# Performance work log

Measured on AMD Instinct MI355X. Metric: run time of the kernel, lower is better.

Reference implementation:

```python
import jax, jax.numpy as jnp
import numpy as np

B, T, N, D, TXT, TE, H = 8, 8192, 256, 512, 768, 2048, 8
DH = D // H


def _ln(x, g, b):
    m = jnp.mean(x, axis=-1, keepdims=True)
    v = jnp.mean(jnp.square(x - m), axis=-1, keepdims=True)
    return (x - m) * jax.lax.rsqrt(v + 1e-5) * g + b


def setup_inputs() -> dict:
    key = jax.random.key(0)
    ks = jax.random.split(key, 10)
    s = 0.02  # init scale for weights (zero_module init replaced by small random for a non-trivial baseline)
    return {
        "x": jax.random.normal(ks[0], (B, T, D), jnp.float32),
        "xf": jax.random.normal(ks[1], (B, N, TXT), jnp.float32),
        "emb": jax.random.normal(ks[2], (B, TE), jnp.float32),
        "ln_x_g": jnp.ones((D,), jnp.float32),
        "ln_x_b": jnp.zeros((D,), jnp.float32),
        "ln_t_g": jnp.ones((TXT,), jnp.float32),
        "ln_t_b": jnp.zeros((TXT,), jnp.float32),
        "Wq": jax.random.normal(ks[3], (D, D), jnp.float32) * s,
        "bq": jnp.zeros((D,), jnp.float32),
        "Wk": jax.random.normal(ks[4], (TXT, D), jnp.float32) * s,
        "bk": jnp.zeros((D,), jnp.float32),
        "Wv": jax.random.normal(ks[5], (TXT, D), jnp.float32) * s,
        "bv": jnp.zeros((D,), jnp.float32),
        "emb_W": jax.random.normal(ks[6], (TE, 2 * D), jnp.float32) * s,
        "emb_b": jnp.zeros((2 * D,), jnp.float32),
        "ln_o_g": jnp.ones((D,), jnp.float32),
        "ln_o_b": jnp.zeros((D,), jnp.float32),
        "out_W": jax.random.normal(ks[7], (D, D), jnp.float32) * s,
        "out_b": jnp.zeros((D,), jnp.float32),
    }


def reference(x, xf, emb, ln_x_g, ln_x_b, ln_t_g, ln_t_b, Wq, bq, Wk, bk, Wv, bv,
              emb_W, emb_b, ln_o_g, ln_o_b, out_W, out_b):
    xt = _ln(xf, ln_t_g, ln_t_b)                                  # [B,N,TXT]
    q = jax.nn.softmax((_ln(x, ln_x_g, ln_x_b) @ Wq + bq).reshape(B, T, H, DH), axis=-1)
    k = jax.nn.softmax((xt @ Wk + bk).reshape(B, N, H, DH), axis=-1)
    v = (xt @ Wv + bv).reshape(B, N, H, DH)
    attn = jnp.einsum('bnhd,bnhl->bhdl', k, v)                    # [B,H,DH,DH] kv aggregation
    out = jnp.einsum('bthd,bhdl->bthl', q, attn).reshape(B, T, D)  # [B,T,D]
    # StylizationBlock
    eo = (jax.nn.silu(emb) @ emb_W + emb_b)[:, None, :]           # [B,1,2D]
    scale, shift = jnp.split(eo, 2, axis=2)
    h = _ln(out, ln_o_g, ln_o_b) * (1 + scale) + shift
    h = jax.nn.silu(h) @ out_W + out_b
    return x + h
```

## Files before the change

### kernel.cpp

```cpp
#include <hip/hip_runtime.h>
#include <hip/hip_bf16.h>
#include <math.h>

#define Bc 8
#define Tc 8192
#define NTOK 256
#define Dc 512
#define TXT 768
#define TEc 2048
#define Hc 8
#define DHc 64
#define MROWS (Bc * Tc)

typedef __attribute__((ext_vector_type(8))) short bf16x8v;
typedef __attribute__((ext_vector_type(8))) unsigned short u16x8;
typedef __attribute__((ext_vector_type(4))) unsigned short u16x4;
typedef __attribute__((ext_vector_type(4))) float f32x4;

#define MFMA16(a, b, c) __builtin_amdgcn_mfma_f32_16x16x32_bf16(a, b, c, 0, 0, 0)

__device__ __forceinline__ unsigned short f2bf(float f) {
    __hip_bfloat16 h = __float2bfloat16(f);
    return __builtin_bit_cast(unsigned short, h);
}
__device__ __forceinline__ float bf2f(unsigned short u) {
    unsigned int x = ((unsigned int)u) << 16;
    return __builtin_bit_cast(float, x);
}

typedef __attribute__((address_space(3))) unsigned int lds_u32_t;
typedef __attribute__((address_space(1))) const unsigned int gbl_u32_t;
__device__ __forceinline__ void gload16(const unsigned short* g, short* l) {
    __builtin_amdgcn_global_load_lds((gbl_u32_t*)g, (lds_u32_t*)l, 16, 0, 0);
}

__global__ void __launch_bounds__(256) transpose_kernel(const float* __restrict__ src,
                                                        unsigned short* __restrict__ dst,
                                                        int N, int rs) {
    __shared__ float tile[64][65];
    int k0 = blockIdx.x * 64, n0 = blockIdx.y * 64;
    int tx = threadIdx.x & 63, tq = threadIdx.x >> 6;
#pragma unroll
    for (int i = 0; i < 16; ++i) {
        int kk = tq + i * 4;
        tile[kk][tx] = src[(size_t)(k0 + kk) * N + n0 + tx];
    }
    __syncthreads();
#pragma unroll
    for (int i = 0; i < 16; ++i) {
        int nn = tq + i * 4;
        dst[(size_t)(n0 + nn) * rs + k0 + tx] = f2bf(tile[tx][nn]);
    }
}

__global__ void __launch_bounds__(256) ln_t_kernel(const float* __restrict__ xf,
                                                   const float* __restrict__ g,
                                                   const float* __restrict__ bt,
                                                   unsigned short* __restrict__ xt) {
    int w = threadIdx.x >> 6, l = threadIdx.x & 63;
    int row = blockIdx.x * 4 + w;
    const float* src = xf + (size_t)row * TXT;
    float4 a0 = *(const float4*)&src[l * 12];
    float4 a1 = *(const float4*)&src[l * 12 + 4];
    float4 a2 = *(const float4*)&src[l * 12 + 8];
    float vals[12] = {a0.x, a0.y, a0.z, a0.w, a1.x, a1.y, a1.z, a1.w,
                      a2.x, a2.y, a2.z, a2.w};
    float s = 0.f, ss = 0.f;
#pragma unroll
    for (int j = 0; j < 12; ++j) { s += vals[j]; ss += vals[j] * vals[j]; }
#pragma unroll
    for (int m = 1; m <= 32; m <<= 1) { s += __shfl_xor(s, m); ss += __shfl_xor(ss, m); }
    float mean = s * (1.f / TXT), var = ss * (1.f / TXT) - mean * mean;
    float rs = rsqrtf(var + 1e-5f);
    unsigned short o[12];
#pragma unroll
    for (int j = 0; j < 12; ++j) {
        int c = l * 12 + j;
        o[j] = f2bf((vals[j] - mean) * rs * g[c] + bt[c]);
    }
    unsigned short* dp = xt + (size_t)row * TXT + l * 12;
    *(u16x4*)&dp[0] = *(u16x4*)&o[0];
    *(u16x4*)&dp[4] = *(u16x4*)&o[4];
    *(u16x4*)&dp[8] = *(u16x4*)&o[8];
}

__global__ void __launch_bounds__(256) ln_x_kernel(const float* __restrict__ x,
                                                   const float* __restrict__ g,
                                                   const float* __restrict__ bt,
                                                   unsigned short* __restrict__ A1) {
    int w = threadIdx.x >> 6, l = threadIdx.x & 63;
    int row = blockIdx.x * 4 + w;
    const float* src = x + (size_t)row * Dc;
    float4 a0 = *(const float4*)&src[l * 8];
    float4 a1 = *(const float4*)&src[l * 8 + 4];
    float vals[8] = {a0.x, a0.y, a0.z, a0.w, a1.x, a1.y, a1.z, a1.w};
    float s = 0.f, ss = 0.f;
#pragma unroll
    for (int j = 0; j < 8; ++j) { s += vals[j]; ss += vals[j] * vals[j]; }
#pragma unroll
    for (int m = 1; m <= 32; m <<= 1) { s += __shfl_xor(s, m); ss += __shfl_xor(ss, m); }
    float mean = s * (1.f / Dc), var = ss * (1.f / Dc) - mean * mean;
    float rs = rsqrtf(var + 1e-5f);
    u16x8 o;
#pragma unroll
    for (int j = 0; j < 8; ++j) {
        int c = l * 8 + j;
        o[j] = f2bf((vals[j] - mean) * rs * g[c] + bt[c]);
    }
    *(u16x8*)&A1[(size_t)row * Dc + l * 8] = o;
}

__global__ void __launch_bounds__(256) kvgemm_kernel(
    const unsigned short* __restrict__ xt, const unsigned short* __restrict__ Wkvt,
    const float* __restrict__ bk, const float* __restrict__ bv,
    unsigned short* __restrict__ kbuf, unsigned short* __restrict__ vbuf) {
    __shared__ short lds_s[16384];
    short* Alds = lds_s;
    short* Blds = lds_s + 8192;

    const int tid = threadIdx.x, l = tid & 63, w = tid >> 6;
    const int lr = l & 15, lg = l >> 4;
    int mt = blockIdx.x >> 3, nt = blockIdx.x & 7;
    int row0 = mt * 128, col0 = nt * 128;
    int wrow = (w >> 1) * 64, wcol = (w & 1) * 64;

    f32x4 acc[4][4] = {};
    const int cbase = w * 64 + l;

    for (int ks = 0; ks < 12; ++ks) {
#pragma unroll
        for (int i = 0; i < 4; ++i) {
            int c = i * 256 + cbase;
            int r = c >> 3, kc = c & 7;
            int koff = ks * 64 + ((kc ^ (r & 7)) << 3);
            gload16(xt + (size_t)(row0 + r) * TXT + koff, &Alds[((i * 4 + w) * 64) * 8]);
            gload16(Wkvt + (size_t)(col0 + r) * TXT + koff, &Blds[((i * 4 + w) * 64) * 8]);
        }
        __syncthreads();
#pragma unroll
        for (int kk = 0; kk < 2; ++kk) {
            int kcw = kk * 4 + lg;
            bf16x8v af[4], bfr[4];
#pragma unroll
            for (int i = 0; i < 4; ++i) {
                int r = wrow + i * 16 + lr;
                af[i] = *(bf16x8v*)&Alds[(r * 8 + (kcw ^ (r & 7))) * 8];
            }
#pragma unroll
            for (int j = 0; j < 4; ++j) {
                int n = wcol + j * 16 + lr;
                bfr[j] = *(bf16x8v*)&Blds[(n * 8 + (kcw ^ (n & 7))) * 8];
            }
#pragma unroll
            for (int i = 0; i < 4; ++i)
#pragma unroll
                for (int j = 0; j < 4; ++j)
                    acc[i][j] = MFMA16(af[i], bfr[j], acc[i][j]);
        }
        __syncthreads();
    }

    const bool kHalf = (col0 + wcol) < 512;
    int cj[4];
    float bias[4];
#pragma unroll
    for (int j = 0; j < 4; ++j) {
        cj[j] = col0 + wcol + j * 16 + lr;
        bias[j] = kHalf ? bk[cj[j]] : bv[cj[j] - 512];
    }
#pragma unroll
    for (int i = 0; i < 4; ++i)
#pragma unroll
        for (int reg = 0; reg < 4; ++reg) {
            float v0 = acc[i][0][reg] + bias[0], v1 = acc[i][1][reg] + bias[1];
            float v2 = acc[i][2][reg] + bias[2], v3 = acc[i][3][reg] + bias[3];
            if (kHalf) {
                float m = fmaxf(fmaxf(v0, v1), fmaxf(v2, v3));
                m = fmaxf(m, __shfl_xor(m, 1)); m = fmaxf(m, __shfl_xor(m, 2));
                m = fmaxf(m, __shfl_xor(m, 4)); m = fmaxf(m, __shfl_xor(m, 8));
                float e0 = __expf(v0 - m), e1 = __expf(v1 - m);
                float e2 = __expf(v2 - m), e3 = __expf(v3 - m);
                float ssum = e0 + e1 + e2 + e3;
                ssum += __shfl_xor(ssum, 1); ssum += __shfl_xor(ssum, 2);
                ssum += __shfl_xor(ssum, 4); ssum += __shfl_xor(ssum, 8);
                float inv = 1.f / ssum;
                v0 = e0 * inv; v1 = e1 * inv; v2 = e2 * inv; v3 = e3 * inv;
            }
            int r = row0 + wrow + i * 16 + 4 * lg + reg;
            float vv[4] = {v0, v1, v2, v3};
#pragma unroll
            for (int j = 0; j < 4; ++j) {
                if (kHalf) kbuf[(size_t)r * Dc + cj[j]] = f2bf(vv[j]);
                else       vbuf[(size_t)r * Dc + cj[j] - 512] = f2bf(vv[j]);
            }
        }
}

__global__ void attn_kernel(const unsigned short* __restrict__ kbuf,
                            const unsigned short* __restrict__ vbuf,
                            unsigned short* __restrict__ attn_t) {
    __shared__ float ks[16][DHc], vs[16][DHc];
    const int tid = threadIdx.x;
    const int b = blockIdx.x >> 3, h = blockIdx.x & 7;
    const int d = tid >> 2, lb = (tid & 3) * 16;
    float acc[16] = {0.f};
    for (int nt = 0; nt < 16; ++nt) {
        __syncthreads();
#pragma unroll
        for (int j = 0; j < 4; ++j) {
            int idx = tid + 256 * j;
            int nn = idx >> 6, cc = idx & 63;
            size_t o = (size_t)(b * NTOK + nt * 16 + nn) * Dc + h * DHc + cc;
            ks[nn][cc] = bf2f(kbuf[o]);
            vs[nn][cc] = bf2f(vbuf[o]);
        }
        __syncthreads();
#pragma unroll
        for (int nn = 0; nn < 16; ++nn) {
            float kd = ks[nn][d];
#pragma unroll
            for (int i = 0; i < 16; ++i) acc[i] += kd * vs[nn][lb + i];
        }
    }
    size_t base = (size_t)(b * 8 + h) * DHc * DHc;
#pragma unroll
    for (int i = 0; i < 16; ++i)
        attn_t[base + (size_t)(lb + i) * DHc + d] = f2bf(acc[i]);
}

__global__ void __launch_bounds__(256) emb_kernel(const float* __restrict__ emb,
                                                  const float* __restrict__ emb_W,
                                                  const float* __restrict__ emb_b,
                                                  float* __restrict__ eo) {
    __shared__ float s[TEc];
    __shared__ float red[4][64];
    const int tid = threadIdx.x;
    const int b = blockIdx.x >> 4, chunk = blockIdx.x & 15;
#pragma unroll
    for (int j = 0; j < 8; ++j) {
        int idx = tid + 256 * j;
        float e = emb[b * TEc + idx];
        s[idx] = e / (1.f + __expf(-e));
    }
    __syncthreads();
    int c = tid & 63, q = tid >> 6;
    int col = chunk * 64 + c;
    float acc = 0.f;
    for (int kk = q * 512; kk < q * 512 + 512; ++kk)
        acc += s[kk] * emb_W[(size_t)kk * (2 * Dc) + col];
    red[q][c] = acc;
    __syncthreads();
    if (q == 0)
        eo[b * (2 * Dc) + col] = red[0][c] + red[1][c] + red[2][c] + red[3][c] + emb_b[col];
}

__global__ void __launch_bounds__(256) gemm1_kernel(
    const unsigned short* __restrict__ A1, const unsigned short* __restrict__ Wt,
    const float* __restrict__ bq, const unsigned short* __restrict__ attn_t,
    unsigned short* __restrict__ out1) {
    __shared__ short lds_s[16384];
    short* Alds = lds_s;
    short* Blds = lds_s + 8192;

    const int tid = threadIdx.x, l = tid & 63, w = tid >> 6;
    const int lr = l & 15, lg = l >> 4;
    int raw = blockIdx.x;
    int swz = (raw & 7) * 256 + (raw >> 3);
    int mt = swz >> 2, nt = swz & 3;
    int row0 = mt * 128, col0 = nt * 128;
    int b = row0 >> 13;
    int wrow = (w >> 1) * 64, wcol = (w & 1) * 64;

    f32x4 acc[4][4] = {};
    const int cbase = w * 64 + l;

    for (int ks = 0; ks < 8; ++ks) {
#pragma unroll
        for (int i = 0; i < 4; ++i) {
            int c = i * 256 + cbase;
            int r = c >> 3, kc = c & 7;
            int koff = ks * 64 + ((kc ^ (r & 7)) << 3);
            gload16(A1 + (size_t)(row0 + r) * Dc + koff, &Alds[((i * 4 + w) * 64) * 8]);
            gload16(Wt + (size_t)(col0 + r) * Dc + koff, &Blds[((i * 4 + w) * 64) * 8]);
        }
        __syncthreads();
#pragma unroll
        for (int kk = 0; kk < 2; ++kk) {
            int kcw = kk * 4 + lg;
            bf16x8v af[4], bfr[4];
#pragma unroll
            for (int i = 0; i < 4; ++i) {
                int r = wrow + i * 16 + lr;
                af[i] = *(bf16x8v*)&Alds[(r * 8 + (kcw ^ (r & 7))) * 8];
            }
#pragma unroll
            for (int j = 0; j < 4; ++j) {
                int n = wcol + j * 16 + lr;
                bfr[j] = *(bf16x8v*)&Blds[(n * 8 + (kcw ^ (n & 7))) * 8];
            }
#pragma unroll
            for (int i = 0; i < 4; ++i)
#pragma unroll
                for (int j = 0; j < 4; ++j)
                    acc[i][j] = MFMA16(af[i], bfr[j], acc[i][j]);
        }
        __syncthreads();
    }

    float bqv[4];
#pragma unroll
    for (int j = 0; j < 4; ++j) bqv[j] = bq[col0 + wcol + j * 16 + lr];
#pragma unroll
    for (int i = 0; i < 4; ++i)
#pragma unroll
        for (int reg = 0; reg < 4; ++reg) {
            float v0 = acc[i][0][reg] + bqv[0], v1 = acc[i][1][reg] + bqv[1];
            float v2 = acc[i][2][reg] + bqv[2], v3 = acc[i][3][reg] + bqv[3];
            float m = fmaxf(fmaxf(v0, v1), fmaxf(v2, v3));
            m = fmaxf(m, __shfl_xor(m, 1)); m = fmaxf(m, __shfl_xor(m, 2));
            m = fmaxf(m, __shfl_xor(m, 4)); m = fmaxf(m, __shfl_xor(m, 8));
            float e0 = __expf(v0 - m), e1 = __expf(v1 - m);
            float e2 = __expf(v2 - m), e3 = __expf(v3 - m);
            float ssum = e0 + e1 + e2 + e3;
            ssum += __shfl_xor(ssum, 1); ssum += __shfl_xor(ssum, 2);
            ssum += __shfl_xor(ssum, 4); ssum += __shfl_xor(ssum, 8);
            float inv = 1.f / ssum;
            acc[i][0][reg] = e0 * inv; acc[i][1][reg] = e1 * inv;
            acc[i][2][reg] = e2 * inv; acc[i][3][reg] = e3 * inv;
        }

    short* qlds = lds_s;
#pragma unroll
    for (int i = 0; i < 4; ++i)
#pragma unroll
        for (int j = 0; j < 4; ++j)
#pragma unroll
            for (int reg = 0; reg < 4; ++reg) {
                int r = wrow + i * 16 + 4 * lg + reg;
                int c = wcol + j * 16 + lr;
                qlds[(r * 16 + ((c >> 3) ^ (r & 7))) * 8 + (c & 7)] = (short)f2bf(acc[i][j][reg]);
            }
    __syncthreads();

    int hw = nt * 2 + (wcol >> 6);
    const unsigned short* at = attn_t + (size_t)(b * 8 + hw) * DHc * DHc;
    bf16x8v bf2[4][2];
#pragma unroll
    for (int j = 0; j < 4; ++j)
#pragma unroll
        for (int kk = 0; kk < 2; ++kk)
            bf2[j][kk] = *(const bf16x8v*)&at[(j * 16 + lr) * DHc + kk * 32 + lg * 8];

    f32x4 acc2[4][4] = {};
#pragma unroll
    for (int kk = 0; kk < 2; ++kk) {
        int kcw = (wcol >> 3) + kk * 4 + lg;
#pragma unroll
        for (int i = 0; i < 4; ++i) {
            int r = wrow + i * 16 + lr;
            bf16x8v a = *(bf16x8v*)&qlds[(r * 16 + (kcw ^ (r & 7))) * 8];
#pragma unroll
            for (int j = 0; j < 4; ++j)
                acc2[i][j] = MFMA16(a, bf2[j][kk], acc2[i][j]);
        }
    }

#pragma unroll
    for (int i = 0; i < 4; ++i)
#pragma unroll
        for (int j = 0; j < 4; ++j)
#pragma unroll
            for (int reg = 0; reg < 4; ++reg) {
                int r = row0 + wrow + i * 16 + 4 * lg + reg;
                int c = col0 + wcol + j * 16 + lr;
                out1[(size_t)r * Dc + c] = f2bf(acc2[i][j][reg]);
            }
}

__global__ void __launch_bounds__(256) mid_kernel(const unsigned short* __restrict__ out1,
                                                  const float* __restrict__ eo,
                                                  const float* __restrict__ g,
                                                  const float* __restrict__ bt,
                                                  unsigned short* __restrict__ A2) {
    int w = threadIdx.x >> 6, l = threadIdx.x & 63;
    int row = blockIdx.x * 4 + w;
    int b = row >> 13;
    u16x8 iv = *(const u16x8*)&out1[(size_t)row * Dc + l * 8];
    float vals[8];
    float s = 0.f, ss = 0.f;
#pragma unroll
    for (int j = 0; j < 8; ++j) {
        vals[j] = bf2f(iv[j]);
        s += vals[j]; ss += vals[j] * vals[j];
    }
#pragma unroll
    for (int m = 1; m <= 32; m <<= 1) { s += __shfl_xor(s, m); ss += __shfl_xor(ss, m); }
    float mean = s * (1.f / Dc), var = ss * (1.f / Dc) - mean * mean;
    float rs = rsqrtf(var + 1e-5f);
    const float* scl = eo + (size_t)b * (2 * Dc);
    const float* shf = scl + Dc;
    u16x8 o;
#pragma unroll
    for (int j = 0; j < 8; ++j) {
        int c = l * 8 + j;
        float t = (vals[j] - mean) * rs * g[c] + bt[c];
        t = t * (1.f + scl[c]) + shf[c];
        t = t / (1.f + __expf(-t));
        o[j] = f2bf(t);
    }
    *(u16x8*)&A2[(size_t)row * Dc + l * 8] = o;
}

__global__ void __launch_bounds__(256) gemm2_kernel(
    const unsigned short* __restrict__ A2, const unsigned short* __restrict__ Wt,
    const float* __restrict__ ob, const float* __restrict__ x,
    float* __restrict__ out) {
    __shared__ short lds_s[16384];
    short* Alds = lds_s;
    short* Blds = lds_s + 8192;

    const int tid = threadIdx.x, l = tid & 63, w = tid >> 6;
    const int lr = l & 15, lg = l >> 4;
    int raw = blockIdx.x;
    int swz = (raw & 7) * 256 + (raw >> 3);
    int mt = swz >> 2, nt = swz & 3;
    int row0 = mt * 128, col0 = nt * 128;
    int wrow = (w >> 1) * 64, wcol = (w & 1) * 64;

    f32x4 acc[4][4] = {};
    const int cbase = w * 64 + l;

    for (int ks = 0; ks < 8; ++ks) {
#pragma unroll
        for (int i = 0; i < 4; ++i) {
            int c = i * 256 + cbase;
            int r = c >> 3, kc = c & 7;
            int koff = ks * 64 + ((kc ^ (r & 7)) << 3);
            gload16(A2 + (size_t)(row0 + r) * Dc + koff, &Alds[((i * 4 + w) * 64) * 8]);
            gload16(Wt + (size_t)(col0 + r) * Dc + koff, &Blds[((i * 4 + w) * 64) * 8]);
        }
        __syncthreads();
#pragma unroll
        for (int kk = 0; kk < 2; ++kk) {
            int kcw = kk * 4 + lg;
            bf16x8v af[4], bfr[4];
#pragma unroll
            for (int i = 0; i < 4; ++i) {
                int r = wrow + i * 16 + lr;
                af[i] = *(bf16x8v*)&Alds[(r * 8 + (kcw ^ (r & 7))) * 8];
            }
#pragma unroll
            for (int j = 0; j < 4; ++j) {
                int n = wcol + j * 16 + lr;
                bfr[j] = *(bf16x8v*)&Blds[(n * 8 + (kcw ^ (n & 7))) * 8];
            }
#pragma unroll
            for (int i = 0; i < 4; ++i)
#pragma unroll
                for (int j = 0; j < 4; ++j)
                    acc[i][j] = MFMA16(af[i], bfr[j], acc[i][j]);
        }
        __syncthreads();
    }

    float obv[4];
#pragma unroll
    for (int j = 0; j < 4; ++j) obv[j] = ob[col0 + wcol + j * 16 + lr];
#pragma unroll
    for (int i = 0; i < 4; ++i)
#pragma unroll
        for (int j = 0; j < 4; ++j)
#pragma unroll
            for (int reg = 0; reg < 4; ++reg) {
                int r = row0 + wrow + i * 16 + 4 * lg + reg;
                int c = col0 + wcol + j * 16 + lr;
                size_t o = (size_t)r * Dc + c;
                out[o] = acc[i][j][reg] + obv[j] + x[o];
            }
}

extern "C" void kernel_launch(void* const* d_in, const int* in_sizes, int n_in,
                              void* d_out, int out_size, void* d_ws, size_t ws_size,
                              hipStream_t stream) {
    const float* x      = (const float*)d_in[0];
    const float* xf     = (const float*)d_in[1];
    const float* emb    = (const float*)d_in[2];
    const float* ln_x_g = (const float*)d_in[3];
    const float* ln_x_b = (const float*)d_in[4];
    const float* ln_t_g = (const float*)d_in[5];
    const float* ln_t_b = (const float*)d_in[6];
    const float* Wq     = (const float*)d_in[7];
    const float* bq     = (const float*)d_in[8];
    const float* Wk     = (const float*)d_in[9];
    const float* bk     = (const float*)d_in[10];
    const float* Wv     = (const float*)d_in[11];
    const float* bv     = (const float*)d_in[12];
    const float* emb_W  = (const float*)d_in[13];
    const float* emb_b  = (const float*)d_in[14];
    const float* ln_o_g = (const float*)d_in[15];
    const float* ln_o_b = (const float*)d_in[16];
    const float* out_W  = (const float*)d_in[17];
    const float* out_b  = (const float*)d_in[18];
    float* out = (float*)d_out;

    unsigned short* xt   = (unsigned short*)d_ws;
    unsigned short* kbuf = xt + (size_t)2048 * TXT;
    unsigned short* vbuf = kbuf + (size_t)2048 * 512;
    unsigned short* Wkvt = vbuf + (size_t)2048 * 512;
    unsigned short* Wqt  = Wkvt + (size_t)1024 * TXT;
    unsigned short* oWt  = Wqt + (size_t)512 * 512;
    unsigned short* attn_t = oWt + (size_t)512 * 512;
    float* eo = (float*)(attn_t + (size_t)64 * 64 * 64);
    unsigned short* A1 = (unsigned short*)(eo + 8 * 1024);
    unsigned short* A2 = A1;
    unsigned short* out1 = (unsigned short*)d_out;

    hipLaunchKernelGGL(transpose_kernel, dim3(8, 8), dim3(256), 0, stream, Wq, Wqt, Dc, Dc);
    hipLaunchKernelGGL(transpose_kernel, dim3(8, 8), dim3(256), 0, stream, out_W, oWt, Dc, Dc);
    hipLaunchKernelGGL(transpose_kernel, dim3(12, 8), dim3(256), 0, stream, Wk, Wkvt, Dc, TXT);
    hipLaunchKernelGGL(transpose_kernel, dim3(12, 8), dim3(256), 0, stream,
                       Wv, Wkvt + (size_t)512 * TXT, Dc, TXT);

    hipLaunchKernelGGL(ln_t_kernel, dim3(NTOK * Bc / 4), dim3(256), 0, stream,
                       xf, ln_t_g, ln_t_b, xt);
    hipLaunchKernelGGL(ln_x_kernel, dim3(MROWS / 4), dim3(256), 0, stream, x, ln_x_g, ln_x_b, A1);
    hipLaunchKernelGGL(kvgemm_kernel, dim3(16 * 8), dim3(256), 0, stream,
                       xt, Wkvt, bk, bv, kbuf, vbuf);
    hipLaunchKernelGGL(attn_kernel, dim3(Bc * Hc), dim3(256), 0, stream, kbuf, vbuf, attn_t);
    hipLaunchKernelGGL(emb_kernel, dim3(Bc * 16), dim3(256), 0, stream, emb, emb_W, emb_b, eo);
    hipLaunchKernelGGL(gemm1_kernel, dim3(MROWS / 128 * 4), dim3(256), 0, stream,
                       A1, Wqt, bq, attn_t, out1);
    hipLaunchKernelGGL(mid_kernel, dim3(MROWS / 4), dim3(256), 0, stream,
                       out1, eo, ln_o_g, ln_o_b, A2);
    hipLaunchKernelGGL(gemm2_kernel, dim3(MROWS / 128 * 4), dim3(256), 0, stream,
                       A2, oWt, out_b, x, out);
}
```

Baseline: 314.6 us.

## Fuse layernorms into full-width GEMM kernels and merge prep launches

Merges the four weight transposes and the text layernorm into one prep kernel. The x layernorm moves into the Q GEMM prologue, and the mid layernorm/modulation/SiLU moves into the output GEMM, each block holding a full 128x512 row tile in LDS. B fragments are now read straight from global memory. The attention aggregation and embedding kernels are also restructured. This removes intermediate round-trips through global memory and several launches, at the cost of one block per CU, large LDS use, and no LDS staging for weights.

New measurement: 483.9 us. 1.54x slower.

```diff
diff --git a/kernel.cpp b/kernel.cpp
--- a/kernel.cpp
+++ b/kernel.cpp
@@ -34,11 +34,10 @@
     __builtin_amdgcn_global_load_lds((gbl_u32_t*)g, (lds_u32_t*)l, 16, 0, 0);
 }
 
-__global__ void __launch_bounds__(256) transpose_kernel(const float* __restrict__ src,
-                                                        unsigned short* __restrict__ dst,
-                                                        int N, int rs) {
+__device__ __forceinline__ void transpose_tile(const float* __restrict__ src,
+                                               unsigned short* __restrict__ dst,
+                                               int N, int rs, int k0, int n0) {
     __shared__ float tile[64][65];
-    int k0 = blockIdx.x * 64, n0 = blockIdx.y * 64;
     int tx = threadIdx.x & 63, tq = threadIdx.x >> 6;
 #pragma unroll
     for (int i = 0; i < 16; ++i) {
@@ -53,12 +52,35 @@
     }
 }
 
-__global__ void __launch_bounds__(256) ln_t_kernel(const float* __restrict__ xf,
-                                                   const float* __restrict__ g,
-                                                   const float* __restrict__ bt,
-                                                   unsigned short* __restrict__ xt) {
+__global__ void __launch_bounds__(256) prep_kernel(
+    const float* __restrict__ Wq, const float* __restrict__ oW,
+    const float* __restrict__ Wk, const float* __restrict__ Wv,
+    const float* __restrict__ xf, const float* __restrict__ ln_t_g,
+    const float* __restrict__ ln_t_b,
+    unsigned short* __restrict__ Wqt, unsigned short* __restrict__ oWt,
+    unsigned short* __restrict__ Wkvt, unsigned short* __restrict__ xt) {
+    int bid = blockIdx.x;
+    if (bid < 64) {
+        transpose_tile(Wq, Wqt, Dc, Dc, (bid >> 3) * 64, (bid & 7) * 64);
+        return;
+    }
+    if (bid < 128) {
+        int i = bid - 64;
+        transpose_tile(oW, oWt, Dc, Dc, (i >> 3) * 64, (i & 7) * 64);
+        return;
+    }
+    if (bid < 224) {
+        int i = bid - 128;
+        transpose_tile(Wk, Wkvt, Dc, TXT, (i >> 3) * 64, (i & 7) * 64);
+        return;
+    }
+    if (bid < 320) {
+        int i = bid - 224;
+        transpose_tile(Wv, Wkvt + (size_t)512 * TXT, Dc, TXT, (i >> 3) * 64, (i & 7) * 64);
+        return;
+    }
     int w = threadIdx.x >> 6, l = threadIdx.x & 63;
-    int row = blockIdx.x * 4 + w;
+    int row = (bid - 320) * 4 + w;
     const float* src = xf + (size_t)row * TXT;
     float4 a0 = *(const float4*)&src[l * 12];
     float4 a1 = *(const float4*)&src[l * 12 + 4];
@@ -76,38 +98,12 @@
 #pragma unroll
     for (int j = 0; j < 12; ++j) {
         int c = l * 12 + j;
-        o[j] = f2bf((vals[j] - mean) * rs * g[c] + bt[c]);
+        o[j] = f2bf((vals[j] - mean) * rs * ln_t_g[c] + ln_t_b[c]);
     }
     unsigned short* dp = xt + (size_t)row * TXT + l * 12;
     *(u16x4*)&dp[0] = *(u16x4*)&o[0];
     *(u16x4*)&dp[4] = *(u16x4*)&o[4];
     *(u16x4*)&dp[8] = *(u16x4*)&o[8];
-}
-
-__global__ void __launch_bounds__(256) ln_x_kernel(const float* __restrict__ x,
-                                                   const float* __restrict__ g,
-                                                   const float* __restrict__ bt,
-                                                   unsigned short* __restrict__ A1) {
-    int w = threadIdx.x >> 6, l = threadIdx.x & 63;
-    int row = blockIdx.x * 4 + w;
-    const float* src = x + (size_t)row * Dc;
-    float4 a0 = *(const float4*)&src[l * 8];
-    float4 a1 = *(const float4*)&src[l * 8 + 4];
-    float vals[8] = {a0.x, a0.y, a0.z, a0.w, a1.x, a1.y, a1.z, a1.w};
-    float s = 0.f, ss = 0.f;
-#pragma unroll
-    for (int j = 0; j < 8; ++j) { s += vals[j]; ss += vals[j] * vals[j]; }
-#pragma unroll
-    for (int m = 1; m <= 32; m <<= 1) { s += __shfl_xor(s, m); ss += __shfl_xor(ss, m); }
-    float mean = s * (1.f / Dc), var = ss * (1.f / Dc) - mean * mean;
-    float rs = rsqrtf(var + 1e-5f);
-    u16x8 o;
-#pragma unroll
-    for (int j = 0; j < 8; ++j) {
-        int c = l * 8 + j;
-        o[j] = f2bf((vals[j] - mean) * rs * g[c] + bt[c]);
-    }
-    *(u16x8*)&A1[(size_t)row * Dc + l * 8] = o;
 }
 
 __global__ void __launch_bounds__(256) kvgemm_kernel(
@@ -196,287 +192,296 @@
         }
 }
 
-__global__ void attn_kernel(const unsigned short* __restrict__ kbuf,
-                            const unsigned short* __restrict__ vbuf,
-                            unsigned short* __restrict__ attn_t) {
-    __shared__ float ks[16][DHc], vs[16][DHc];
+__global__ void __launch_bounds__(512) attn_kernel(const unsigned short* __restrict__ kbuf,
+                                                   const unsigned short* __restrict__ vbuf,
+                                                   unsigned short* __restrict__ attn_t) {
+    __shared__ unsigned short ksh[128][DHc], vsh[128][DHc];
     const int tid = threadIdx.x;
     const int b = blockIdx.x >> 3, h = blockIdx.x & 7;
-    const int d = tid >> 2, lb = (tid & 3) * 16;
-    float acc[16] = {0.f};
-    for (int nt = 0; nt < 16; ++nt) {
+    const int d = tid >> 3, lb = (tid & 7) * 8;
+    const int tok = tid >> 2, c0 = (tid & 3) * 16;
+    float acc[8] = {0.f};
+    for (int st = 0; st < 2; ++st) {
         __syncthreads();
-#pragma unroll
-        for (int j = 0; j < 4; ++j) {
-            int idx = tid + 256 * j;
-            int nn = idx >> 6, cc = idx & 63;
-            size_t o = (size_t)(b * NTOK + nt * 16 + nn) * Dc + h * DHc + cc;
-            ks[nn][cc] = bf2f(kbuf[o]);
-            vs[nn][cc] = bf2f(vbuf[o]);
-        }
+        size_t o = (size_t)(b * NTOK + st * 128 + tok) * Dc + h * DHc + c0;
+        *(u16x8*)&ksh[tok][c0]     = *(const u16x8*)&kbuf[o];
+        *(u16x8*)&ksh[tok][c0 + 8] = *(const u16x8*)&kbuf[o + 8];
+        *(u16x8*)&vsh[tok][c0]     = *(const u16x8*)&vbuf[o];
+        *(u16x8*)&vsh[tok][c0 + 8] = *(const u16x8*)&vbuf[o + 8];
         __syncthreads();
-#pragma unroll
-        for (int nn = 0; nn < 16; ++nn) {
-            float kd = ks[nn][d];
-#pragma unroll
-            for (int i = 0; i < 16; ++i) acc[i] += kd * vs[nn][lb + i];
+        for (int n = 0; n < 128; ++n) {
+            float kd = bf2f(ksh[n][d]);
+            u16x4 va = *(const u16x4*)&vsh[n][lb];
+            u16x4 vb = *(const u16x4*)&vsh[n][lb + 4];
+#pragma unroll
+            for (int e = 0; e < 4; ++e) acc[e] += kd * bf2f(va[e]);
+#pragma unroll
+            for (int e = 0; e < 4; ++e) acc[4 + e] += kd * bf2f(vb[e]);
         }
     }
     size_t base = (size_t)(b * 8 + h) * DHc * DHc;
 #pragma unroll
-    for (int i = 0; i < 16; ++i)
-        attn_t[base + (size_t)(lb + i) * DHc + d] = f2bf(acc[i]);
+    for (int e = 0; e < 8; ++e)
+        attn_t[base + (size_t)(lb + e) * DHc + d] = f2bf(acc[e]);
 }
 
 __global__ void __launch_bounds__(256) emb_kernel(const float* __restrict__ emb,
                                                   const float* __restrict__ emb_W,
                                                   const float* __restrict__ emb_b,
                                                   float* __restrict__ eo) {
-    __shared__ float s[TEc];
-    __shared__ float red[4][64];
+    __shared__ float s[4][TEc];
+    __shared__ float red[4][64][4];
     const int tid = threadIdx.x;
-    const int b = blockIdx.x >> 4, chunk = blockIdx.x & 15;
+    const int chunk = blockIdx.x >> 1, bh = blockIdx.x & 1;
 #pragma unroll
     for (int j = 0; j < 8; ++j) {
         int idx = tid + 256 * j;
-        float e = emb[b * TEc + idx];
-        s[idx] = e / (1.f + __expf(-e));
+        int bi = idx >> 9, kk4 = (idx & 511) * 4;
+#pragma unroll
+        for (int e = 0; e < 4; ++e) {
+            float v = emb[(bh * 4 + bi) * TEc + kk4 + e];
+            s[bi][kk4 + e] = v / (1.f + __expf(-v));
+        }
     }
     __syncthreads();
     int c = tid & 63, q = tid >> 6;
     int col = chunk * 64 + c;
-    float acc = 0.f;
-    for (int kk = q * 512; kk < q * 512 + 512; ++kk)
-        acc += s[kk] * emb_W[(size_t)kk * (2 * Dc) + col];
-    red[q][c] = acc;
+    float acc[4] = {0.f, 0.f, 0.f, 0.f};
+    for (int kk = q * 512; kk < q * 512 + 512; ++kk) {
+        float wv = emb_W[(size_t)kk * (2 * Dc) + col];
+#pragma unroll
+        for (int bi = 0; bi < 4; ++bi) acc[bi] += s[bi][kk] * wv;
+    }
+#pragma unroll
+    for (int bi = 0; bi < 4; ++bi) red[q][c][bi] = acc[bi];
     __syncthreads();
-    if (q == 0)
-        eo[b * (2 * Dc) + col] = red[0][c] + red[1][c] + red[2][c] + red[3][c] + emb_b[col];
-}
-
-__global__ void __launch_bounds__(256) gemm1_kernel(
-    const unsigned short* __restrict__ A1, const unsigned short* __restrict__ Wt,
+    if (q == 0) {
+        float bb = emb_b[col];
+#pragma unroll
+        for (int bi = 0; bi < 4; ++bi)
+            eo[(bh * 4 + bi) * (2 * Dc) + col] =
+                red[0][c][bi] + red[1][c][bi] + red[2][c][bi] + red[3][c][bi] + bb;
+    }
+}
+
+__global__ void __launch_bounds__(512, 1) gemm1m_kernel(
+    const float* __restrict__ x, const float* __restrict__ lng,
+    const float* __restrict__ lnb, const unsigned short* __restrict__ Wt,
     const float* __restrict__ bq, const unsigned short* __restrict__ attn_t,
     unsigned short* __restrict__ out1) {
-    __shared__ short lds_s[16384];
-    short* Alds = lds_s;
-    short* Blds = lds_s + 8192;
-
+    __shared__ short lds_s[73728];
+    short* A = lds_s;
     const int tid = threadIdx.x, l = tid & 63, w = tid >> 6;
     const int lr = l & 15, lg = l >> 4;
-    int raw = blockIdx.x;
-    int swz = (raw & 7) * 256 + (raw >> 3);
-    int mt = swz >> 2, nt = swz & 3;
-    int row0 = mt * 128, col0 = nt * 128;
-    int b = row0 >> 13;
-    int wrow = (w >> 1) * 64, wcol = (w & 1) * 64;
-
-    f32x4 acc[4][4] = {};
-    const int cbase = w * 64 + l;
-
-    for (int ks = 0; ks < 8; ++ks) {
+    short* Qw = lds_s + 65536 + w * 1024;
+
+    const int row0 = blockIdx.x * 128;
+    const int b = row0 >> 13;
+    const int wrow = (w >> 2) * 64, wcol = (w & 3) * 64;
+
+    {
+        float4 g0 = *(const float4*)&lng[l * 8], g1 = *(const float4*)&lng[l * 8 + 4];
+        float4 b0 = *(const float4*)&lnb[l * 8], b1 = *(const float4*)&lnb[l * 8 + 4];
+        float gg[8] = {g0.x, g0.y, g0.z, g0.w, g1.x, g1.y, g1.z, g1.w};
+        float bb[8] = {b0.x, b0.y, b0.z, b0.w, b1.x, b1.y, b1.z, b1.w};
+        for (int rr = 0; rr < 16; ++rr) {
+            int r = w * 16 + rr;
+            const float* src = x + (size_t)(row0 + r) * Dc + l * 8;
+            float4 a0 = *(const float4*)&src[0];
+            float4 a1 = *(const float4*)&src[4];
+            float vals[8] = {a0.x, a0.y, a0.z, a0.w, a1.x, a1.y, a1.z, a1.w};
+            float s = 0.f, ss = 0.f;
+#pragma unroll
+            for (int j = 0; j < 8; ++j) { s += vals[j]; ss += vals[j] * vals[j]; }
+#pragma unroll
+            for (int m = 1; m <= 32; m <<= 1) { s += __shfl_xor(s, m); ss += __shfl_xor(ss, m); }
+            float mean = s * (1.f / Dc), var = ss * (1.f / Dc) - mean * mean;
+            float rsq = rsqrtf(var + 1e-5f);
+            bf16x8v o;
+#pragma unroll
+            for (int j = 0; j < 8; ++j)
+                o[j] = (short)f2bf((vals[j] - mean) * rsq * gg[j] + bb[j]);
+            *(bf16x8v*)&A[((size_t)r * 64 + (l ^ (r & 7))) * 8] = o;
+        }
+    }
+    __syncthreads();
+
+    for (int nt = 0; nt < 2; ++nt) {
+        const int col0 = nt * 256;
+        f32x4 acc[4][4] = {};
+#pragma unroll
+        for (int ks = 0; ks < 8; ++ks) {
+#pragma unroll
+            for (int kk = 0; kk < 2; ++kk) {
+                int kcw = ks * 8 + kk * 4 + lg;
+                bf16x8v af[4], bfr[4];
+#pragma unroll
+                for (int i = 0; i < 4; ++i) {
+                    int r = wrow + i * 16 + lr;
+                    af[i] = *(bf16x8v*)&A[((size_t)r * 64 + (kcw ^ (r & 7))) * 8];
+                }
+#pragma unroll
+                for (int j = 0; j < 4; ++j)
+                    bfr[j] = *(const bf16x8v*)&Wt[(size_t)(col0 + wcol + j * 16 + lr) * Dc + kcw * 8];
+#pragma unroll
+                for (int i = 0; i < 4; ++i)
+#pragma unroll
+                    for (int j = 0; j < 4; ++j)
+                        acc[i][j] = MFMA16(af[i], bfr[j], acc[i][j]);
+            }
+        }
+
+        float bqv[4];
+#pragma unroll
+        for (int j = 0; j < 4; ++j) bqv[j] = bq[col0 + wcol + j * 16 + lr];
+
+        int hw = nt * 4 + (w & 3);
+        const unsigned short* at = attn_t + (size_t)(b * 8 + hw) * DHc * DHc;
+        bf16x8v bf2[4][2];
+#pragma unroll
+        for (int j = 0; j < 4; ++j)
+#pragma unroll
+            for (int kk = 0; kk < 2; ++kk)
+                bf2[j][kk] = *(const bf16x8v*)&at[(j * 16 + lr) * DHc + kk * 32 + lg * 8];
+
 #pragma unroll
         for (int i = 0; i < 4; ++i) {
-            int c = i * 256 + cbase;
-            int r = c >> 3, kc = c & 7;
-            int koff = ks * 64 + ((kc ^ (r & 7)) << 3);
-            gload16(A1 + (size_t)(row0 + r) * Dc + koff, &Alds[((i * 4 + w) * 64) * 8]);
-            gload16(Wt + (size_t)(col0 + r) * Dc + koff, &Blds[((i * 4 + w) * 64) * 8]);
-        }
-        __syncthreads();
-#pragma unroll
-        for (int kk = 0; kk < 2; ++kk) {
-            int kcw = kk * 4 + lg;
-            bf16x8v af[4], bfr[4];
-#pragma unroll
-            for (int i = 0; i < 4; ++i) {
-                int r = wrow + i * 16 + lr;
-                af[i] = *(bf16x8v*)&Alds[(r * 8 + (kcw ^ (r & 7))) * 8];
-            }
-#pragma unroll
-            for (int j = 0; j < 4; ++j) {
-                int n = wcol + j * 16 + lr;
-                bfr[j] = *(bf16x8v*)&Blds[(n * 8 + (kcw ^ (n & 7))) * 8];
-            }
-#pragma unroll
-            for (int i = 0; i < 4; ++i)
+#pragma unroll
+            for (int reg = 0; reg < 4; ++reg) {
+                float v0 = acc[i][0][reg] + bqv[0], v1 = acc[i][1][reg] + bqv[1];
+                float v2 = acc[i][2][reg] + bqv[2], v3 = acc[i][3][reg] + bqv[3];
+                float m = fmaxf(fmaxf(v0, v1), fmaxf(v2, v3));
+                m = fmaxf(m, __shfl_xor(m, 1)); m = fmaxf(m, __shfl_xor(m, 2));
+                m = fmaxf(m, __shfl_xor(m, 4)); m = fmaxf(m, __shfl_xor(m, 8));
+                float e0 = __expf(v0 - m), e1 = __expf(v1 - m);
+                float e2 = __expf(v2 - m), e3 = __expf(v3 - m);
+                float ssum = e0 + e1 + e2 + e3;
+                ssum += __shfl_xor(ssum, 1); ssum += __shfl_xor(ssum, 2);
+                ssum += __shfl_xor(ssum, 4); ssum += __shfl_xor(ssum, 8);
+                float inv = 1.f / ssum;
+                acc[i][0][reg] = e0 * inv; acc[i][1][reg] = e1 * inv;
+                acc[i][2][reg] = e2 * inv; acc[i][3][reg] = e3 * inv;
+            }
+#pragma unroll
+            for (int j = 0; j < 4; ++j)
+#pragma unroll
+                for (int reg = 0; reg < 4; ++reg) {
+                    int rl = 4 * lg + reg;
+                    int c = j * 16 + lr;
+                    Qw[(rl * 8 + ((c >> 3) ^ (rl & 7))) * 8 + (c & 7)] =
+                        (short)f2bf(acc[i][j][reg]);
+                }
+            f32x4 acc2[4] = {};
+#pragma unroll
+            for (int kk = 0; kk < 2; ++kk) {
+                int kc = kk * 4 + lg;
+                bf16x8v a = *(bf16x8v*)&Qw[(lr * 8 + (kc ^ (lr & 7))) * 8];
 #pragma unroll
                 for (int j = 0; j < 4; ++j)
-                    acc[i][j] = MFMA16(af[i], bfr[j], acc[i][j]);
-        }
-        __syncthreads();
-    }
-
-    float bqv[4];
-#pragma unroll
-    for (int j = 0; j < 4; ++j) bqv[j] = bq[col0 + wcol + j * 16 + lr];
-#pragma unroll
-    for (int i = 0; i < 4; ++i)
-#pragma unroll
-        for (int reg = 0; reg < 4; ++reg) {
-            float v0 = acc[i][0][reg] + bqv[0], v1 = acc[i][1][reg] + bqv[1];
-            float v2 = acc[i][2][reg] + bqv[2], v3 = acc[i][3][reg] + bqv[3];
-            float m = fmaxf(fmaxf(v0, v1), fmaxf(v2, v3));
-            m = fmaxf(m, __shfl_xor(m, 1)); m = fmaxf(m, __shfl_xor(m, 2));
-            m = fmaxf(m, __shfl_xor(m, 4)); m = fmaxf(m, __shfl_xor(m, 8));
-            float e0 = __expf(v0 - m), e1 = __expf(v1 - m);
-            float e2 = __expf(v2 - m), e3 = __expf(v3 - m);
-            float ssum = e0 + e1 + e2 + e3;
-            ssum += __shfl_xor(ssum, 1); ssum += __shfl_xor(ssum, 2);
-            ssum += __shfl_xor(ssum, 4); ssum += __shfl_xor(ssum, 8);
-            float inv = 1.f / ssum;
-            acc[i][0][reg] = e0 * inv; acc[i][1][reg] = e1 * inv;
-            acc[i][2][reg] = e2 * inv; acc[i][3][reg] = e3 * inv;
-        }
-
-    short* qlds = lds_s;
-#pragma unroll
-    for (int i = 0; i < 4; ++i)
-#pragma unroll
-        for (int j = 0; j < 4; ++j)
-#pragma unroll
-            for (int reg = 0; reg < 4; ++reg) {
-                int r = wrow + i * 16 + 4 * lg + reg;
-                int c = wcol + j * 16 + lr;
-                qlds[(r * 16 + ((c >> 3) ^ (r & 7))) * 8 + (c & 7)] = (short)f2bf(acc[i][j][reg]);
-            }
-    __syncthreads();
-
-    int hw = nt * 2 + (wcol >> 6);
-    const unsigned short* at = attn_t + (size_t)(b * 8 + hw) * DHc * DHc;
-    bf16x8v bf2[4][2];
-#pragma unroll
-    for (int j = 0; j < 4; ++j)
-#pragma unroll
-        for (int kk = 0; kk < 2; ++kk)
-            bf2[j][kk] = *(const bf16x8v*)&at[(j * 16 + lr) * DHc + kk * 32 + lg * 8];
-
-    f32x4 acc2[4][4] = {};
-#pragma unroll
-    for (int kk = 0; kk < 2; ++kk) {
-        int kcw = (wcol >> 3) + kk * 4 + lg;
-#pragma unroll
-        for (int i = 0; i < 4; ++i) {
-            int r = wrow + i * 16 + lr;
-            bf16x8v a = *(bf16x8v*)&qlds[(r * 16 + (kcw ^ (r & 7))) * 8];
+                    acc2[j] = MFMA16(a, bf2[j][kk], acc2[j]);
+            }
 #pragma unroll
             for (int j = 0; j < 4; ++j)
-                acc2[i][j] = MFMA16(a, bf2[j][kk], acc2[i][j]);
-        }
-    }
-
-#pragma unroll
-    for (int i = 0; i < 4; ++i)
-#pragma unroll
-        for (int j = 0; j < 4; ++j)
-#pragma unroll
-            for (int reg = 0; reg < 4; ++reg) {
-                int r = row0 + wrow + i * 16 + 4 * lg + reg;
-                int c = col0 + wcol + j * 16 + lr;
-                out1[(size_t)r * Dc + c] = f2bf(acc2[i][j][reg]);
-            }
-}
-
-__global__ void __launch_bounds__(256) mid_kernel(const unsigned short* __restrict__ out1,
-                                                  const float* __restrict__ eo,
-                                                  const float* __restrict__ g,
-                                                  const float* __restrict__ bt,
-                                                  unsigned short* __restrict__ A2) {
-    int w = threadIdx.x >> 6, l = threadIdx.x & 63;
-    int row = blockIdx.x * 4 + w;
-    int b = row >> 13;
-    u16x8 iv = *(const u16x8*)&out1[(size_t)row * Dc + l * 8];
-    float vals[8];
-    float s = 0.f, ss = 0.f;
-#pragma unroll
-    for (int j = 0; j < 8; ++j) {
-        vals[j] = bf2f(iv[j]);
-        s += vals[j]; ss += vals[j] * vals[j];
-    }
-#pragma unroll
-    for (int m = 1; m <= 32; m <<= 1) { s += __shfl_xor(s, m); ss += __shfl_xor(ss, m); }
-    float mean = s * (1.f / Dc), var = ss * (1.f / Dc) - mean * mean;
-    float rs = rsqrtf(var + 1e-5f);
-    const float* scl = eo + (size_t)b * (2 * Dc);
-    const float* shf = scl + Dc;
-    u16x8 o;
-#pragma unroll
-    for (int j = 0; j < 8; ++j) {
-        int c = l * 8 + j;
-        float t = (vals[j] - mean) * rs * g[c] + bt[c];
-        t = t * (1.f + scl[c]) + shf[c];
-        t = t / (1.f + __expf(-t));
-        o[j] = f2bf(t);
-    }
-    *(u16x8*)&A2[(size_t)row * Dc + l * 8] = o;
-}
-
-__global__ void __launch_bounds__(256) gemm2_kernel(
-    const unsigned short* __restrict__ A2, const unsigned short* __restrict__ Wt,
-    const float* __restrict__ ob, const float* __restrict__ x,
-    float* __restrict__ out) {
-    __shared__ short lds_s[16384];
-    short* Alds = lds_s;
-    short* Blds = lds_s + 8192;
-
+#pragma unroll
+                for (int reg = 0; reg < 4; ++reg) {
+                    int r = row0 + wrow + i * 16 + 4 * lg + reg;
+                    int c = col0 + wcol + j * 16 + lr;
+                    out1[(size_t)r * Dc + c] = f2bf(acc2[j][reg]);
+                }
+        }
+    }
+}
+
+__global__ void __launch_bounds__(512, 1) gemm2m_kernel(
+    const unsigned short* __restrict__ out1, const float* __restrict__ eo,
+    const float* __restrict__ lng, const float* __restrict__ lnb,
+    const unsigned short* __restrict__ Wt, const float* __restrict__ ob,
+    const float* __restrict__ x, float* __restrict__ out) {
+    __shared__ short lds_s[65536];
+    short* A = lds_s;
     const int tid = threadIdx.x, l = tid & 63, w = tid >> 6;
     const int lr = l & 15, lg = l >> 4;
-    int raw = blockIdx.x;
-    int swz = (raw & 7) * 256 + (raw >> 3);
-    int mt = swz >> 2, nt = swz & 3;
-    int row0 = mt * 128, col0 = nt * 128;
-    int wrow = (w >> 1) * 64, wcol = (w & 1) * 64;
-
-    f32x4 acc[4][4] = {};
-    const int cbase = w * 64 + l;
-
-    for (int ks = 0; ks < 8; ++ks) {
-#pragma unroll
-        for (int i = 0; i < 4; ++i) {
-            int c = i * 256 + cbase;
-            int r = c >> 3, kc = c & 7;
-            int koff = ks * 64 + ((kc ^ (r & 7)) << 3);
-            gload16(A2 + (size_t)(row0 + r) * Dc + koff, &Alds[((i * 4 + w) * 64) * 8]);
-            gload16(Wt + (size_t)(col0 + r) * Dc + koff, &Blds[((i * 4 + w) * 64) * 8]);
-        }
-        __syncthreads();
-#pragma unroll
-        for (int kk = 0; kk < 2; ++kk) {
-            int kcw = kk * 4 + lg;
-            bf16x8v af[4], bfr[4];
-#pragma unroll
-            for (int i = 0; i < 4; ++i) {
-                int r = wrow + i * 16 + lr;
-                af[i] = *(bf16x8v*)&Alds[(r * 8 + (kcw ^ (r & 7))) * 8];
-            }
-#pragma unroll
-            for (int j = 0; j < 4; ++j) {
-                int n = wcol + j * 16 + lr;
-                bfr[j] = *(bf16x8v*)&Blds[(n * 8 + (kcw ^ (n & 7))) * 8];
-            }
-#pragma unroll
-            for (int i = 0; i < 4; ++i)
+
+    const int row0 = blockIdx.x * 128;
+    const int b = row0 >> 13;
+    const int wrow = (w >> 2) * 64, wcol = (w & 3) * 64;
+
+    {
+        float4 g0 = *(const float4*)&lng[l * 8], g1 = *(const float4*)&lng[l * 8 + 4];
+        float4 b0 = *(const float4*)&lnb[l * 8], b1 = *(const float4*)&lnb[l * 8 + 4];
+        const float* scl = eo + (size_t)b * (2 * Dc);
+        const float* shf = scl + Dc;
+        float4 s0 = *(const float4*)&scl[l * 8], s1 = *(const float4*)&scl[l * 8 + 4];
+        float4 h0 = *(const float4*)&shf[l * 8], h1 = *(const float4*)&shf[l * 8 + 4];
+        float gg[8] = {g0.x, g0.y, g0.z, g0.w, g1.x, g1.y, g1.z, g1.w};
+        float bb[8] = {b0.x, b0.y, b0.z, b0.w, b1.x, b1.y, b1.z, b1.w};
+        float sc[8] = {s0.x, s0.y, s0.z, s0.w, s1.x, s1.y, s1.z, s1.w};
+        float sh[8] = {h0.x, h0.y, h0.z, h0.w, h1.x, h1.y, h1.z, h1.w};
+        for (int rr = 0; rr < 16; ++rr) {
+            int r = w * 16 + rr;
+            u16x8 iv = *(const u16x8*)&out1[(size_t)(row0 + r) * Dc + l * 8];
+            float vals[8];
+            float s = 0.f, ss = 0.f;
+#pragma unroll
+            for (int j = 0; j < 8; ++j) {
+                vals[j] = bf2f(iv[j]);
+                s += vals[j]; ss += vals[j] * vals[j];
+            }
+#pragma unroll
+            for (int m = 1; m <= 32; m <<= 1) { s += __shfl_xor(s, m); ss += __shfl_xor(ss, m); }
+            float mean = s * (1.f / Dc), var = ss * (1.f / Dc) - mean * mean;
+            float rsq = rsqrtf(var + 1e-5f);
+            bf16x8v o;
+#pragma unroll
+            for (int j = 0; j < 8; ++j) {
+                float t = (vals[j] - mean) * rsq * gg[j] + bb[j];
+                t = t * (1.f + sc[j]) + sh[j];
+                o[j] = (short)f2bf(t / (1.f + __expf(-t)));
+            }
+            *(bf16x8v*)&A[((size_t)r * 64 + (l ^ (r & 7))) * 8] = o;
+        }
+    }
+    __syncthreads();
+
+    for (int nt = 0; nt < 2; ++nt) {
+        const int col0 = nt * 256;
+        f32x4 acc[4][4] = {};
+#pragma unroll
+        for (int ks = 0; ks < 8; ++ks) {
+#pragma unroll
+            for (int kk = 0; kk < 2; ++kk) {
+                int kcw = ks * 8 + kk * 4 + lg;
+                bf16x8v af[4], bfr[4];
+#pragma unroll
+                for (int i = 0; i < 4; ++i) {
+                    int r = wrow + i * 16 + lr;
+                    af[i] = *(bf16x8v*)&A[((size_t)r * 64 + (kcw ^ (r & 7))) * 8];
+                }
 #pragma unroll
                 for (int j = 0; j < 4; ++j)
-                    acc[i][j] = MFMA16(af[i], bfr[j], acc[i][j]);
-        }
-        __syncthreads();
-    }
-
-    float obv[4];
-#pragma unroll
-    for (int j = 0; j < 4; ++j) obv[j] = ob[col0 + wcol + j * 16 + lr];
-#pragma unroll
-    for (int i = 0; i < 4; ++i)
-#pragma unroll
-        for (int j = 0; j < 4; ++j)
-#pragma unroll
-            for (int reg = 0; reg < 4; ++reg) {
-                int r = row0 + wrow + i * 16 + 4 * lg + reg;
-                int c = col0 + wcol + j * 16 + lr;
-                size_t o = (size_t)r * Dc + c;
-                out[o] = acc[i][j][reg] + obv[j] + x[o];
-            }
+                    bfr[j] = *(const bf16x8v*)&Wt[(size_t)(col0 + wcol + j * 16 + lr) * Dc + kcw * 8];
+#pragma unroll
+                for (int i = 0; i < 4; ++i)
+#pragma unroll
+                    for (int j = 0; j < 4; ++j)
+                        acc[i][j] = MFMA16(af[i], bfr[j], acc[i][j]);
+            }
+        }
+        float obv[4];
+#pragma unroll
+        for (int j = 0; j < 4; ++j) obv[j] = ob[col0 + wcol + j * 16 + lr];
+#pragma unroll
+        for (int i = 0; i < 4; ++i)
+#pragma unroll
+            for (int j = 0; j < 4; ++j)
+#pragma unroll
+                for (int reg = 0; reg < 4; ++reg) {
+                    int r = row0 + wrow + i * 16 + 4 * lg + reg;
+                    int c = col0 + wcol + j * 16 + lr;
+                    size_t o = (size_t)r * Dc + c;
+                    out[o] = acc[i][j][reg] + obv[j] + x[o];
+                }
+    }
 }
 
 extern "C" void kernel_launch(void* const* d_in, const int* in_sizes, int n_in,
@@ -511,27 +516,17 @@
     unsigned short* oWt  = Wqt + (size_t)512 * 512;
     unsigned short* attn_t = oWt + (size_t)512 * 512;
     float* eo = (float*)(attn_t + (size_t)64 * 64 * 64);
-    unsigned short* A1 = (unsigned short*)(eo + 8 * 1024);
-    unsigned short* A2 = A1;
-    unsigned short* out1 = (unsigned short*)d_out;
-
-    hipLaunchKernelGGL(transpose_kernel, dim3(8, 8), dim3(256), 0, stream, Wq, Wqt, Dc, Dc);
-    hipLaunchKernelGGL(transpose_kernel, dim3(8, 8), dim3(256), 0, stream, out_W, oWt, Dc, Dc);
-    hipLaunchKernelGGL(transpose_kernel, dim3(12, 8), dim3(256), 0, stream, Wk, Wkvt, Dc, TXT);
-    hipLaunchKernelGGL(transpose_kernel, dim3(12, 8), dim3(256), 0, stream,
-                       Wv, Wkvt + (size_t)512 * TXT, Dc, TXT);
-
-    hipLaunchKernelGGL(ln_t_kernel, dim3(NTOK * Bc / 4), dim3(256), 0, stream,
-                       xf, ln_t_g, ln_t_b, xt);
-    hipLaunchKernelGGL(ln_x_kernel, dim3(MROWS / 4), dim3(256), 0, stream, x, ln_x_g, ln_x_b, A1);
+    unsigned short* out1 = (unsigned short*)(eo + 8 * 1024);
+
+    hipLaunchKernelGGL(prep_kernel, dim3(832), dim3(256), 0, stream,
+                       Wq, out_W, Wk, Wv, xf, ln_t_g, ln_t_b, Wqt, oWt, Wkvt, xt);
     hipLaunchKernelGGL(kvgemm_kernel, dim3(16 * 8), dim3(256), 0, stream,
                        xt, Wkvt, bk, bv, kbuf, vbuf);
-    hipLaunchKernelGGL(attn_kernel, dim3(Bc * Hc), dim3(256), 0, stream, kbuf, vbuf, attn_t);
-    hipLaunchKernelGGL(emb_kernel, dim3(Bc * 16), dim3(256), 0, stream, emb, emb_W, emb_b, eo);
-    hipLaunchKernelGGL(gemm1_kernel, dim3(MROWS / 128 * 4), dim3(256), 0, stream,
-                       A1, Wqt, bq, attn_t, out1);
-    hipLaunchKernelGGL(mid_kernel, dim3(MROWS / 4), dim3(256), 0, stream,
-                       out1, eo, ln_o_g, ln_o_b, A2);
-    hipLaunchKernelGGL(gemm2_kernel, dim3(MROWS / 128 * 4), dim3(256), 0, stream,
-                       A2, oWt, out_b, x, out);
-}
+    hipLaunchKernelGGL(attn_kernel, dim3(Bc * Hc), dim3(512), 0, stream,
+                       kbuf, vbuf, attn_t);
+    hipLaunchKernelGGL(emb_kernel, dim3(32), dim3(256), 0, stream, emb, emb_W, emb_b, eo);
+    hipLaunchKernelGGL(gemm1m_kernel, dim3(MROWS / 128), dim3(512), 0, stream,
+                       x, ln_x_g, ln_x_b, Wqt, bq, attn_t, out1);
+    hipLaunchKernelGGL(gemm2m_kernel, dim3(MROWS / 128), dim3(512), 0, stream,
+                       out1, eo, ln_o_g, ln_o_b, oWt, out_b, x, out);
+}
```
